# Kernel tuning notes

Hardware: AMD Instinct MI355X
Metric: run time of the kernel (lower is better)

Reference implementation:

```python
import jax, jax.numpy as jnp
import numpy as np

B, H, N, D, HID, NIT = 8, 16, 2048, 64, 256, 4
LR = 1.0


def setup_inputs() -> dict:
    key = jax.random.key(0)
    kq, kk, kv, k1, k2 = jax.random.split(key, 5)
    q = jax.random.normal(kq, (B, H, N, D), jnp.float32)
    k = jax.random.normal(kk, (B, H, N, D), jnp.float32)
    v = jax.random.normal(kv, (B, H, N, D), jnp.float32)
    # xavier_uniform per-head init for the 2-layer inner encoder
    l1 = float(np.sqrt(6.0 / (D + HID)))
    l2 = float(np.sqrt(6.0 / (HID + D)))
    W1 = jax.random.uniform(k1, (H, D, HID), jnp.float32, -l1, l1)
    W2 = jax.random.uniform(k2, (H, HID, D), jnp.float32, -l2, l2)
    return {"q": q, "k": k, "v": v, "W1": W1, "W2": W2, "training": 1, "return_aux": 0}


def _enc(params, x):
    # per-head 2-layer MLP: x (H, M, D) -> (H, M, D); no bias, no LN, no residual
    W1, W2 = params
    h = jax.nn.gelu(jnp.einsum('hmd,hde->hme', x, W1))  # flax nn.gelu = approximate gelu
    return jnp.einsum('hme,heo->hmo', h, W2)


def _inner_loss(params, data):
    x = data[..., :D]
    y = data[..., D:]
    return 0.5 * jnp.mean(jnp.square(y - _enc(params, x))) * H


def reference(q, k, v, W1, W2, training, return_aux):
    ilr = jnp.ones((NIT, H), jnp.float32) * LR
    # train set: inputs=k, targets=v (no inp/trg LN, no trg_proj with out_dim=None)
    data = jnp.concatenate([k, v], axis=-1)  # (B, H, N, 2D)
    chunk = N // NIT
    # split along N into NIT mini-batches, stacked on a scan axis: (B, NIT, H, chunk, 2D)
    data = data.reshape(B, H, NIT, chunk, 2 * D).transpose(0, 2, 1, 3, 4)

    def step(params, ilr_data):
        lr, d = ilr_data  # lr: (H,), d: (H, chunk, 2D)
        _, grads = jax.value_and_grad(_inner_loss)(params, d)
        params = jax.tree_util.tree_map(
            lambda p, g: p - lr.reshape(-1, 1, 1) * g, params, grads)
        return params, None

    # learnable_init=False -> stop_gradient on initial inner params
    init = (jax.lax.stop_gradient(W1), jax.lax.stop_gradient(W2))

    def inner_loop(db):  # db: (NIT, H, chunk, 2D)
        final, _ = jax.lax.scan(step, init, (ilr, db))
        return final

    final_params = jax.vmap(inner_loop)(data)  # leaves have leading B
    test_out = jax.vmap(_enc)(final_params, q)  # (B, H, N, D)
    return test_out.transpose(0, 2, 1, 3).reshape(B, N, H * D)
```

## Files before the change

kernel.cpp:

```cpp
#include <hip/hip_runtime.h>
#include <hip/hip_bf16.h>

typedef __hip_bfloat16 bf16;
typedef __attribute__((ext_vector_type(8))) short frag8;
typedef __attribute__((ext_vector_type(4))) float frag4f;
typedef __attribute__((ext_vector_type(4))) short short4v;

#define BB 8
#define HH 16
#define NTOK 2048
#define DD 64
#define HID 256
#define NIT 4
#define CH 512
#define NP 128
#define INV_CD 3.0517578125e-05f

#define MFMA(a,b,c) __builtin_amdgcn_mfma_f32_16x16x32_bf16((a),(b),(c),0,0,0)

#define SW(row,col) ((col) ^ ((((row)>>3)&3)<<4))

__device__ __forceinline__ short f2b(float f){
    union { __hip_bfloat16 b; short s; } u;
    u.b = __float2bfloat16(f);
    return u.s;
}

__device__ __forceinline__ float tanh_fast(float u){
    float e = __expf(2.0f*u);
    return 1.0f - 2.0f/(e+1.0f);
}

__device__ __forceinline__ float gelu_f(float x){
    const float c0 = 0.7978845608028654f, c1 = 0.044715f;
    float u = c0*(x + c1*x*x*x);
    float t = tanh_fast(u);
    return 0.5f*x*(1.0f+t);
}

__device__ __forceinline__ void gelu_both(float x, float* hv, float* gp){
    const float c0 = 0.7978845608028654f, c1 = 0.044715f;
    float x2 = x*x;
    float u = c0*(x + c1*x2*x);
    float t = tanh_fast(u);
    *hv = 0.5f*x*(1.0f+t);
    *gp = 0.5f*(1.0f+t) + 0.5f*x*(1.0f-t*t)*c0*(1.0f+3.0f*c1*x2);
}

__global__ __launch_bounds__(1024, 4) void k_step(
    const float* __restrict__ kin, const float* __restrict__ vin,
    const float* __restrict__ MoW1, const float* __restrict__ MoW2,
    const float* __restrict__ Pin,  float* __restrict__ Mnew,
    float* __restrict__ Pout, int hIdx, int fold, int t)
{
    int p = blockIdx.x >> 1, half = blockIdx.x & 1;
    int tid = threadIdx.x;
    int w = tid >> 6, lane = tid & 63, q = lane >> 4, ln = lane & 15;
    int s = w >> 2, ch = w & 3;

    __shared__ __attribute__((aligned(16))) short W1c[256*72];
    __shared__ __attribute__((aligned(16))) short W2c[64*264];
    __shared__ __attribute__((aligned(16))) short hl [64*264];
    __shared__ __attribute__((aligned(16))) short el [64*72];
    __shared__ __attribute__((aligned(16))) short eTl[64*72];
    __shared__ __attribute__((aligned(16))) short dzTl[256*72];

    {
        int widx = hIdx ? (p & 15) : p;
        const float* w1o = MoW1 + (size_t)widx*16384;
        const float* w2o = MoW2 + (size_t)widx*16384;
        const float* pa = Pin + (size_t)p*32768;
        const float* pb = Pin + (size_t)(NP+p)*32768;
        float* mn1 = Mnew + (size_t)p*16384;
        float* mn2 = Mnew + (size_t)(NP+p)*16384;
        #pragma unroll 4
        for (int i=0;i<16;i++){
            int src = i*1024 + tid;
            float a = w1o[src];
            float b = w2o[src];
            if (fold){
                a -= pa[src] + pb[src];
                b -= pa[16384+src] + pb[16384+src];
            }
            if (half == 0){
                mn1[src] = a;
                mn2[src] = b;
            }
            W1c[(src & 255)*72  + (src >> 8)] = f2b(a);
            W2c[(src & 63)*264  + SW(src & 63, src >> 6)] = f2b(b);
        }
    }
    __syncthreads();

    frag4f dw1[4], dw2[4];
    #pragma unroll
    for (int i=0;i<4;i++){ frag4f zz = {0.f,0.f,0.f,0.f}; dw1[i]=zz; dw2[i]=zz; }

    size_t rowbase = (size_t)p*NTOK + (size_t)t*CH + (size_t)half*256;

    #pragma unroll 1
    for (int mt=0; mt<4; ++mt){
        int m0 = mt*64;

        frag8 af[2];
        {
            const float* xb = kin + (rowbase + m0 + s*16 + ln)*DD;
            #pragma unroll
            for (int kk=0;kk<2;kk++){
                const float* xr = xb + kk*32 + q*8;
                float4 u0 = *(const float4*)xr;
                float4 u1 = *(const float4*)(xr+4);
                frag8 a;
                a[0]=f2b(u0.x); a[1]=f2b(u0.y); a[2]=f2b(u0.z); a[3]=f2b(u0.w);
                a[4]=f2b(u1.x); a[5]=f2b(u1.y); a[6]=f2b(u1.z); a[7]=f2b(u1.w);
                af[kk]=a;
            }
        }
        frag4f zacc[4];
        #pragma unroll
        for (int nti=0;nti<4;nti++){
            frag4f zc = {0.f,0.f,0.f,0.f};
            #pragma unroll
            for (int kk=0;kk<2;kk++){
                frag8 b = *(const frag8*)&W1c[((ch*4+nti)*16+ln)*72 + kk*32 + q*8];
                zc = MFMA(af[kk], b, zc);
            }
            zacc[nti] = zc;
        }
        #pragma unroll
        for (int nti=0;nti<4;nti++)
            #pragma unroll
            for (int r=0;r<4;r++){
                float hv, gp;
                gelu_both(zacc[nti][r], &hv, &gp);
                int row = s*16+q*4+r;
                hl[row*264 + SW(row, (ch*4+nti)*16 + ln)] = f2b(hv);
                zacc[nti][r] = gp;
            }
        __syncthreads();

        {
            frag8 hfr[8];
            #pragma unroll
            for (int kk=0;kk<8;kk++)
                hfr[kk] = *(const frag8*)&hl[(s*16+ln)*264 + SW(s*16+ln, kk*32 + q*8)];
            frag4f oc = {0.f,0.f,0.f,0.f};
            #pragma unroll
            for (int kk=0;kk<8;kk++){
                frag8 b = *(const frag8*)&W2c[(ch*16+ln)*264 + SW(ch*16+ln, kk*32 + q*8)];
                oc = MFMA(hfr[kk], b, oc);
            }
            short4v ep;
            #pragma unroll
            for (int r=0;r<4;r++){
                float y = vin[(rowbase + m0 + s*16 + q*4 + r)*DD + ch*16 + ln];
                float e = (oc[r]-y)*INV_CD;
                el[(s*16+q*4+r)*72 + ch*16 + ln] = f2b(e);
                ep[r] = f2b(e);
            }
            *(short4v*)&eTl[(ch*16+ln)*72 + s*16 + q*4] = ep;
        }
        __syncthreads();

        {
            frag8 efr[2];
            #pragma unroll
            for (int kk=0;kk<2;kk++)
                efr[kk] = *(const frag8*)&el[(s*16+ln)*72 + kk*32 + q*8];
            #pragma unroll
            for (int nti=0;nti<4;nti++){
                int nt = ch*4 + nti;
                frag4f dc = {0.f,0.f,0.f,0.f};
                #pragma unroll
                for (int kk=0;kk<2;kk++){
                    frag8 b;
                    #pragma unroll
                    for (int j=0;j<8;j++){
                        int row = kk*32+q*8+j;
                        b[j] = W2c[row*264 + SW(row, nt*16 + ln)];
                    }
                    dc = MFMA(efr[kk], b, dc);
                }
                short4v dp;
                #pragma unroll
                for (int r=0;r<4;r++)
                    dp[r] = f2b(dc[r]*zacc[nti][r]);
                *(short4v*)&dzTl[(nt*16+ln)*72 + s*16 + q*4] = dp;
            }
        }
        __syncthreads();

        {
            #pragma unroll
            for (int kk2=0;kk2<2;kk2++){
                frag8 a;
                #pragma unroll
                for (int j=0;j<8;j++)
                    a[j] = f2b(kin[(rowbase + m0 + kk2*32 + q*8 + j)*DD + s*16 + ln]);
                #pragma unroll
                for (int nti=0;nti<4;nti++){
                    frag8 b = *(const frag8*)&dzTl[((ch*4+nti)*16+ln)*72 + kk2*32 + q*8];
                    dw1[nti] = MFMA(a, b, dw1[nti]);
                }
            }
            #pragma unroll
            for (int kk2=0;kk2<2;kk2++){
                frag8 a;
                #pragma unroll
                for (int j=0;j<8;j++){
                    int row = kk2*32+q*8+j;
                    a[j] = hl[row*264 + SW(row, w*16 + ln)];
                }
                #pragma unroll
                for (int ot=0;ot<4;ot++){
                    frag8 b = *(const frag8*)&eTl[(ot*16+ln)*72 + kk2*32 + q*8];
                    dw2[ot] = MFMA(a, b, dw2[ot]);
                }
            }
        }
        __syncthreads();
    }

    {
        float* pw1 = Pout + ((size_t)half*NP + p)*32768;
        float* pw2 = pw1 + 16384;
        #pragma unroll
        for (int nti=0;nti<4;nti++)
            #pragma unroll
            for (int r=0;r<4;r++)
                pw1[(s*16 + q*4 + r)*256 + (ch*4+nti)*16 + ln] = dw1[nti][r];
        #pragma unroll
        for (int ot=0;ot<4;ot++)
            #pragma unroll
            for (int r=0;r<4;r++)
                pw2[(w*16 + q*4 + r)*64 + ot*16 + ln] = dw2[ot][r];
    }
}

__global__ __launch_bounds__(1024) void k_castW(const float* __restrict__ M0,
                                                const float* __restrict__ P1,
                                                short* __restrict__ W1p,
                                                short* __restrict__ W2p){
    int p = blockIdx.x >> 1, which = blockIdx.x & 1;
    int tid = threadIdx.x;
    __shared__ float F[256*65];
    const float* m  = M0 + ((size_t)(which ? NP+p : p))*16384;
    const float* pa = P1 + (size_t)p*32768      + (size_t)which*16384;
    const float* pb = P1 + (size_t)(NP+p)*32768 + (size_t)which*16384;

    #pragma unroll
    for (int i=0;i<4;i++){
        int idx4 = i*4096 + tid*4;
        float4 mv = *(const float4*)(m  + idx4);
        float4 av = *(const float4*)(pa + idx4);
        float4 bv = *(const float4*)(pb + idx4);
        float vv[4] = { mv.x-av.x-bv.x, mv.y-av.y-bv.y, mv.z-av.z-bv.z, mv.w-av.w-bv.w };
        if (which == 0){
            int row = idx4 >> 8, col = idx4 & 255;
            #pragma unroll
            for (int e=0;e<4;e++) F[row*257 + col + e] = vv[e];
        } else {
            int row = idx4 >> 6, col = idx4 & 63;
            #pragma unroll
            for (int e=0;e<4;e++) F[row*65 + col + e] = vv[e];
        }
    }
    __syncthreads();

    #pragma unroll
    for (int inst=0;inst<2;inst++){
        int fi = inst*1024 + tid;
        int slot = fi >> 6, l = fi & 63;
        int qf = l >> 4, lnf = l & 15;
        frag8 v;
        if (which == 0){
            int nt = slot >> 1, kk = slot & 1;
            #pragma unroll
            for (int j=0;j<8;j++)
                v[j] = f2b(F[(kk*32 + qf*8 + j)*257 + nt*16 + lnf]);
            *(frag8*)(W1p + (((size_t)p*32 + slot)*64 + l)*8) = v;
        } else {
            int nt = slot >> 3, kk = slot & 7;
            #pragma unroll
            for (int j=0;j<8;j++)
                v[j] = f2b(F[(kk*32 + qf*8 + j)*65 + nt*16 + lnf]);
            *(frag8*)(W2p + (((size_t)p*32 + slot)*64 + l)*8) = v;
        }
    }
}

__global__ __launch_bounds__(256) void k_apply(const float* __restrict__ qin,
                                               const short* __restrict__ W1p,
                                               const short* __restrict__ W2p,
                                               float* __restrict__ out){
    int p = blockIdx.x >> 5, mt = blockIdx.x & 31;
    int tid = threadIdx.x;
    int w = tid >> 6, lane = tid & 63, q = lane >> 4, ln = lane & 15;
    int m0 = mt*64;
    int b = p >> 4, h = p & 15;
    __shared__ __attribute__((aligned(16))) short hl[64*264];
    float* ol = (float*)hl;
    const float* xbase = qin + ((size_t)p*NTOK + m0 + w*16 + ln)*DD;
    frag8 af[2];
    #pragma unroll
    for (int kk=0;kk<2;kk++){
        const float* xr = xbase + kk*32 + q*8;
        float4 u0 = *(const float4*)xr;
        float4 u1 = *(const float4*)(xr+4);
        frag8 a;
        a[0]=f2b(u0.x); a[1]=f2b(u0.y); a[2]=f2b(u0.z); a[3]=f2b(u0.w);
        a[4]=f2b(u1.x); a[5]=f2b(u1.y); a[6]=f2b(u1.z); a[7]=f2b(u1.w);
        af[kk]=a;
    }
    const short* w1b = W1p + ((size_t)p*32*64 + lane)*8;
    #pragma unroll
    for (int nt=0;nt<16;nt++){
        frag4f zc = {0.f,0.f,0.f,0.f};
        #pragma unroll
        for (int kk=0;kk<2;kk++){
            frag8 bfr = *(const frag8*)(w1b + (size_t)(nt*2+kk)*64*8);
            zc = MFMA(bfr, af[kk], zc);
        }
        short4v hp;
        #pragma unroll
        for (int r=0;r<4;r++)
            hp[r] = f2b(gelu_f(zc[r]));
        *(short4v*)&hl[(w*16+ln)*264 + nt*16 + q*4] = hp;
    }
    __syncthreads();
    frag8 hfr[8];
    #pragma unroll
    for (int kk=0;kk<8;kk++)
        hfr[kk] = *(const frag8*)(&hl[(w*16+ln)*264 + kk*32 + q*8]);
    __syncthreads();
    const short* w2b = W2p + ((size_t)p*32*64 + lane)*8;
    frag4f oc4[4];
    #pragma unroll
    for (int nt=0;nt<4;nt++){
        frag4f oc = {0.f,0.f,0.f,0.f};
        #pragma unroll
        for (int kk=0;kk<8;kk++){
            frag8 bfr = *(const frag8*)(w2b + (size_t)(nt*8+kk)*64*8);
            oc = MFMA(hfr[kk], bfr, oc);
        }
        oc4[nt] = oc;
    }
    #pragma unroll
    for (int nt=0;nt<4;nt++)
        #pragma unroll
        for (int r=0;r<4;r++)
            ol[(w*16+q*4+r)*68 + nt*16 + ln] = oc4[nt][r];
    __syncthreads();
    size_t obase = ((size_t)b*NTOK + m0)*(HH*DD) + (size_t)h*DD;
    int c8 = tid & 7;
    #pragma unroll
    for (int pass=0; pass<2; pass++){
        int row = pass*32 + (tid>>3);
        #pragma unroll
        for (int u=0; u<2; u++){
            float4 vv = *(const float4*)&ol[row*68 + (c8 + u*8)*4];
            *(float4*)&out[obase + (size_t)row*(HH*DD) + (c8 + u*8)*4] = vv;
        }
    }
}

extern "C" void kernel_launch(void* const* d_in, const int* in_sizes, int n_in,
                              void* d_out, int out_size, void* d_ws, size_t ws_size,
                              hipStream_t stream) {
    (void)in_sizes; (void)n_in; (void)out_size; (void)ws_size;
    const float* q  = (const float*)d_in[0];
    const float* k  = (const float*)d_in[1];
    const float* v  = (const float*)d_in[2];
    const float* W1 = (const float*)d_in[3];
    const float* W2 = (const float*)d_in[4];
    float* out = (float*)d_out;

    float* P0  = (float*)d_ws;
    short* W1p = (short*)d_ws;
    short* W2p = W1p + (size_t)NP*16384;

    float* M0 = (float*)d_out;
    float* M1 = M0 + (size_t)NP*32768;
    float* P1 = M1 + (size_t)NP*32768;

    k_step<<<256,1024,0,stream>>>(k, v,  W1,   W2,                        P0,  M1,  P0,  1,   0,  0);
    k_step<<<256,1024,0,stream>>>(k, v,  M1,   M1+(size_t)NP*16384,       P0,  M0,  P1,  0,   1,  1);
    k_step<<<256,1024,0,stream>>>(k, v,  M0,   M0+(size_t)NP*16384,       P1,  M1,  P0,  0,   1,  2);
    k_step<<<256,1024,0,stream>>>(k, v,  M1,   M1+(size_t)NP*16384,       P0,  M0,  P1,  0,   1,  3);
    k_castW<<<NP*2, 1024, 0, stream>>>(M0, P1, W1p, W2p);
    k_apply<<<NP*32, 256, 0, stream>>>(q, W1p, W2p, out);
}
```

Baseline: 500.5 us.

## Prefetch targets early in train kernel and simplify apply kernel stores

Result: faster. 473.5 us (-5.4%).

```diff
diff --git a/kernel.cpp b/kernel.cpp
--- a/kernel.cpp
+++ b/kernel.cpp
@@ -116,6 +116,11 @@
                 af[kk]=a;
             }
         }
+        float yv[4];
+        #pragma unroll
+        for (int r=0;r<4;r++)
+            yv[r] = vin[(rowbase + m0 + s*16 + q*4 + r)*DD + ch*16 + ln];
+
         frag4f zacc[4];
         #pragma unroll
         for (int nti=0;nti<4;nti++){
@@ -153,8 +158,7 @@
             short4v ep;
             #pragma unroll
             for (int r=0;r<4;r++){
-                float y = vin[(rowbase + m0 + s*16 + q*4 + r)*DD + ch*16 + ln];
-                float e = (oc[r]-y)*INV_CD;
+                float e = (oc[r]-yv[r])*INV_CD;
                 el[(s*16+q*4+r)*72 + ch*16 + ln] = f2b(e);
                 ep[r] = f2b(e);
             }
@@ -298,8 +302,7 @@
     int w = tid >> 6, lane = tid & 63, q = lane >> 4, ln = lane & 15;
     int m0 = mt*64;
     int b = p >> 4, h = p & 15;
-    __shared__ __attribute__((aligned(16))) short hl[64*264];
-    float* ol = (float*)hl;
+    __shared__ short hl[64*264];
     const float* xbase = qin + ((size_t)p*NTOK + m0 + w*16 + ln)*DD;
     frag8 af[2];
     #pragma unroll
@@ -319,22 +322,18 @@
         #pragma unroll
         for (int kk=0;kk<2;kk++){
             frag8 bfr = *(const frag8*)(w1b + (size_t)(nt*2+kk)*64*8);
-            zc = MFMA(bfr, af[kk], zc);
-        }
-        short4v hp;
+            zc = MFMA(af[kk], bfr, zc);
+        }
         #pragma unroll
         for (int r=0;r<4;r++)
-            hp[r] = f2b(gelu_f(zc[r]));
-        *(short4v*)&hl[(w*16+ln)*264 + nt*16 + q*4] = hp;
+            hl[(w*16 + q*4 + r)*264 + nt*16 + ln] = f2b(gelu_f(zc[r]));
     }
     __syncthreads();
     frag8 hfr[8];
     #pragma unroll
     for (int kk=0;kk<8;kk++)
         hfr[kk] = *(const frag8*)(&hl[(w*16+ln)*264 + kk*32 + q*8]);
-    __syncthreads();
     const short* w2b = W2p + ((size_t)p*32*64 + lane)*8;
-    frag4f oc4[4];
     #pragma unroll
     for (int nt=0;nt<4;nt++){
         frag4f oc = {0.f,0.f,0.f,0.f};
@@ -343,23 +342,10 @@
             frag8 bfr = *(const frag8*)(w2b + (size_t)(nt*8+kk)*64*8);
             oc = MFMA(hfr[kk], bfr, oc);
         }
-        oc4[nt] = oc;
-    }
-    #pragma unroll
-    for (int nt=0;nt<4;nt++)
-        #pragma unroll
-        for (int r=0;r<4;r++)
-            ol[(w*16+q*4+r)*68 + nt*16 + ln] = oc4[nt][r];
-    __syncthreads();
-    size_t obase = ((size_t)b*NTOK + m0)*(HH*DD) + (size_t)h*DD;
-    int c8 = tid & 7;
-    #pragma unroll
-    for (int pass=0; pass<2; pass++){
-        int row = pass*32 + (tid>>3);
-        #pragma unroll
-        for (int u=0; u<2; u++){
-            float4 vv = *(const float4*)&ol[row*68 + (c8 + u*8)*4];
-            *(float4*)&out[obase + (size_t)row*(HH*DD) + (c8 + u*8)*4] = vv;
+        #pragma unroll
+        for (int r=0;r<4;r++){
+            int n = m0 + w*16 + q*4 + r;
+            out[((size_t)b*NTOK + n)*(HH*DD) + h*DD + nt*16 + ln] = oc[r];
         }
     }
 }
```
